# Optimization experiments

Hardware: AMD Instinct MI355X
Metric: run time of the kernel (lower is better)

Reference implementation:

```python
import jax, jax.numpy as jnp
import numpy as np


def _relative_position_index(ws: int) -> np.ndarray:
    # Matches torch meshgrid (ij) construction in _init_relative_positions.
    coords = np.stack(np.meshgrid(np.arange(ws), np.arange(ws), indexing='ij'), axis=0).reshape(2, -1)  # [2, ws*ws]
    rel = coords[:, :, None] - coords[:, None, :]          # [2, N, N]
    rel = rel.transpose(1, 2, 0).copy()                    # [N, N, 2]
    rel[:, :, 0] += ws - 1
    rel[:, :, 1] += ws - 1
    rel[:, :, 0] *= 2 * ws - 1
    return rel.sum(-1)                                     # [N, N] int


def setup_inputs() -> dict:
    key = jax.random.key(0)
    ks = jax.random.split(key, 6)
    B, N, C, H, WS = 4096, 49, 512, 16, 7
    x = jax.random.normal(ks[0], (B, N, C), dtype=jnp.float32)
    w_qkv = jax.random.normal(ks[1], (C, 3 * C), dtype=jnp.float32) * (C ** -0.5)
    b_qkv = jax.random.normal(ks[2], (3 * C,), dtype=jnp.float32) * 0.02
    w_proj = jax.random.normal(ks[3], (C, C), dtype=jnp.float32) * (C ** -0.5)
    b_proj = jax.random.normal(ks[4], (C,), dtype=jnp.float32) * 0.02
    bias_table = jax.random.normal(ks[5], ((2 * WS - 1) ** 2, H), dtype=jnp.float32) * 0.02
    return {"x": x, "w_qkv": w_qkv, "b_qkv": b_qkv, "w_proj": w_proj,
            "b_proj": b_proj, "bias_table": bias_table,
            "num_heads": H, "window_size": WS}


def reference(x, w_qkv, b_qkv, w_proj, b_proj, bias_table, num_heads, window_size):
    B, N, C = x.shape
    hd = C // num_heads
    qkv = (x @ w_qkv + b_qkv).reshape(B, N, 3, num_heads, hd)
    q, k, v = (qkv[:, :, i].transpose(0, 2, 1, 3) for i in range(3))  # each [B, H, N, hd]
    # NOTE: scale uses full channel dim C (as in source), not head_dim.
    attn = jnp.einsum('bhnd,bhmd->bhnm', q, k) * (C ** -0.5)          # [B, H, N, N]
    idx = _relative_position_index(window_size)                        # [N, N] static
    rel_bias = bias_table[idx].transpose(2, 0, 1)                      # [H, N, N]
    attn = jax.nn.softmax(attn + rel_bias[None], axis=-1)
    out = jnp.einsum('bhnm,bhmd->bhnd', attn, v)                       # [B, H, N, hd]
    out = out.transpose(0, 2, 1, 3).reshape(B, N, C)
    return out @ w_proj + b_proj
```

## Files before the change

### kernel.cpp

```cpp
#include <hip/hip_runtime.h>
#include <hip/hip_bf16.h>

typedef __attribute__((ext_vector_type(8))) short bf16x8;
typedef __attribute__((ext_vector_type(4))) float f32x4;

#define DEVI __device__ __forceinline__

DEVI short f2bf(float f) {
  union { float f; unsigned u; } v; v.f = f;
  unsigned r = v.u + 0x7FFFu + ((v.u >> 16) & 1u);
  return (short)(r >> 16);
}

DEVI void gl16(const void* g, void* l) {
  __builtin_amdgcn_global_load_lds((const __attribute__((address_space(1))) unsigned*)g,
                                   (__attribute__((address_space(3))) unsigned*)l,
                                   16, 0, 0);
}

DEVI float exp2a(float x) { float r; asm("v_exp_f32 %0, %1" : "=v"(r) : "v"(x)); return r; }

DEVI unsigned pk2(float lo, float hi) {
  union { __hip_bfloat162 h; unsigned u; } v;
  float2 f; f.x = lo; f.y = hi;
  v.h = __float22bfloat162_rn(f);
  return v.u;
}

union U8 { unsigned u[4]; bf16x8 v; };
DEVI bf16x8 mk8(unsigned a, unsigned b, unsigned c, unsigned d) {
  U8 x; x.u[0]=a; x.u[1]=b; x.u[2]=c; x.u[3]=d; return x.v;
}


__global__ __launch_bounds__(256) void conv_x_k(const float* __restrict__ x,
                                                short* __restrict__ xb) {
  long i = (long)blockIdx.x * 256 + threadIdx.x;
  const float4* xf = (const float4*)x;
  float4 a = xf[i * 2], c = xf[i * 2 + 1];
  bf16x8 r;
  r[0] = f2bf(a.x); r[1] = f2bf(a.y); r[2] = f2bf(a.z); r[3] = f2bf(a.w);
  r[4] = f2bf(c.x); r[5] = f2bf(c.y); r[6] = f2bf(c.z); r[7] = f2bf(c.w);
  *(bf16x8*)(xb + i * 8) = r;
}

__global__ __launch_bounds__(256) void conv_wT_k(const float* __restrict__ w,
                                                 short* __restrict__ wT, int Ncols) {
  int i = blockIdx.x * 256 + threadIdx.x;
  if (i >= Ncols * 512) return;
  int n = i >> 9, k = i & 511;
  wT[i] = f2bf(w[k * Ncols + n]);
}

__global__ __launch_bounds__(256) void fill_biasT(const float* __restrict__ btab,
                                                  float* __restrict__ biasT) {
  int i = blockIdx.x * 256 + threadIdx.x;
  int h = i >> 12, m = (i >> 6) & 63, n = i & 63;
  float v;
  if (m >= 49) {
    v = -1e30f;
  } else {
    int nn = n > 48 ? 48 : n;
    int ni = nn / 7, nj = nn - ni * 7;
    int mi = m / 7,  mj = m - mi * 7;
    int idx = (ni - mi + 6) * 13 + (nj - mj + 6);
    v = btab[idx * 16 + h] * 1.4426950408889634f;
  }
  biasT[i] = v;
}


template <int EPI>
__global__ __launch_bounds__(512, 2)
void gemm256(const short* __restrict__ A, const short* __restrict__ Bt,
             const float* __restrict__ bias, void* __restrict__ outp, int ctiles) {
  __shared__ short Ls[65536];

  const int nwg = gridDim.x;
  const int w = blockIdx.x;
  const int chunk = nwg >> 3;
  const int tid = (w & 7) * chunk + (w >> 3);
  const int rt = tid / ctiles, ct = tid % ctiles;
  const long m0 = (long)rt * 256;
  const int n0 = ct * 256;

  const int t = threadIdx.x;
  const int lane = t & 63;
  const int wv = t >> 6;
  const int wr = wv >> 2;
  const int wc = wv & 3;
  const int l15 = lane & 15, g = lane >> 4;

  const int srow = t >> 3;
  const int gch = (t & 7) ^ (srow & 7);
  const short* Ag = A + (m0 + srow) * 512 + gch * 8;
  const short* Bg = Bt + (long)(n0 + srow) * 512 + gch * 8;

  const int x7 = l15 & 7;
  const int c0 = (g ^ x7) * 8;
  const int c1 = ((4 + g) ^ x7) * 8;
  const int rA64 = (wr * 128 + l15) * 64;
  const int rB64 = (wc * 64 + l15) * 64 + 16384;

  f32x4 acc[8][4] = {};

  {
    short* Ad = Ls + t * 8;
    short* Bd = Ls + 16384 + t * 8;
#pragma unroll
    for (int s2 = 0; s2 < 4; ++s2) {
      gl16(Ag + s2 * 32768, Ad + s2 * 4096);
      gl16(Bg + s2 * 32768, Bd + s2 * 4096);
    }
  }
  __syncthreads();

  for (int kt = 0; kt < 8; ++kt) {
    const int cur = kt & 1;
    const short* Ab = Ls + cur * 32768;
    short* Ad = Ls + (cur ^ 1) * 32768 + t * 8;
    short* Bd = Ad + 16384;
    const short* Agk = Ag + (kt + 1) * 64;
    const short* Bgk = Bg + (kt + 1) * 64;

    bf16x8 af[8], bf[4];

#pragma unroll
    for (int mf = 0; mf < 8; ++mf) af[mf] = *(const bf16x8*)(Ab + rA64 + mf * 1024 + c0);
#pragma unroll
    for (int nf = 0; nf < 4; ++nf) bf[nf] = *(const bf16x8*)(Ab + rB64 + nf * 1024 + c0);
    if (kt < 7) {
#pragma unroll
      for (int s2 = 0; s2 < 4; ++s2) gl16(Agk + s2 * 32768, Ad + s2 * 4096);
    }
#pragma unroll
    for (int mf = 0; mf < 8; ++mf)
#pragma unroll
      for (int nf = 0; nf < 4; ++nf)
        acc[mf][nf] = __builtin_amdgcn_mfma_f32_16x16x32_bf16(af[mf], bf[nf], acc[mf][nf], 0, 0, 0);

#pragma unroll
    for (int mf = 0; mf < 8; ++mf) af[mf] = *(const bf16x8*)(Ab + rA64 + mf * 1024 + c1);
#pragma unroll
    for (int nf = 0; nf < 4; ++nf) bf[nf] = *(const bf16x8*)(Ab + rB64 + nf * 1024 + c1);
    if (kt < 7) {
#pragma unroll
      for (int s2 = 0; s2 < 4; ++s2) gl16(Bgk + s2 * 32768, Bd + s2 * 4096);
    }
#pragma unroll
    for (int mf = 0; mf < 8; ++mf)
#pragma unroll
      for (int nf = 0; nf < 4; ++nf)
        acc[mf][nf] = __builtin_amdgcn_mfma_f32_16x16x32_bf16(af[mf], bf[nf], acc[mf][nf], 0, 0, 0);

    __syncthreads();
  }

  if (EPI == 0) {
    short* qkv = (short*)outp;
#pragma unroll
    for (int mf = 0; mf < 8; ++mf)
#pragma unroll
      for (int r = 0; r < 4; ++r) {
        int row = (int)m0 + wr * 128 + mf * 16 + g * 4 + r;
        int b = row / 49, n = row - b * 49;
#pragma unroll
        for (int nf = 0; nf < 4; ++nf) {
          int col = n0 + wc * 64 + nf * 16 + l15;
          float val = acc[mf][nf][r] + bias[col];
          int ii = col >> 9, h = (col >> 5) & 15, d = col & 31;
          qkv[(long)((b * 16 + h) * 3 + ii) * 1568 + n * 32 + d] = f2bf(val);
        }
      }
  } else {
    float* out = (float*)outp;
#pragma unroll
    for (int mf = 0; mf < 8; ++mf)
#pragma unroll
      for (int r = 0; r < 4; ++r) {
        long row = m0 + wr * 128 + mf * 16 + g * 4 + r;
#pragma unroll
        for (int nf = 0; nf < 4; ++nf) {
          int col = n0 + wc * 64 + nf * 16 + l15;
          out[row * 512 + col] = acc[mf][nf][r] + bias[col];
        }
      }
  }
}


__global__ __launch_bounds__(256, 3)
void attn49(const short* __restrict__ qkvb, const float* __restrict__ biasT,
            short* __restrict__ ao) {
  const int t = threadIdx.x, lane = t & 63, wv = t >> 6;
  const int l15 = lane & 15, g = lane >> 4, g4 = g * 4;
  const int b = blockIdx.x >> 2;
  const int h = (blockIdx.x & 3) * 4 + wv;

  const short* qb = qkvb + (long)(b * 16 + h) * 3 * 1568;
  const short* kb = qb + 1568;
  const short* vb = kb + 1568;

  bf16x8 qf[4], kf[4];
#pragma unroll
  for (int i = 0; i < 4; ++i) {
    int row = i * 16 + l15; row = row > 48 ? 48 : row;
    kf[i] = *(const bf16x8*)(kb + row * 32 + g * 8);
    qf[i] = *(const bf16x8*)(qb + row * 32 + g * 8);
  }

  bf16x8 vf[2][2];
#pragma unroll
  for (int kt = 0; kt < 2; ++kt)
#pragma unroll
    for (int hi = 0; hi < 2; ++hi)
#pragma unroll
      for (int r = 0; r < 4; ++r) {
        int m = kt * 32 + hi * 16 + g4 + r;
        m = m > 48 ? 48 : m;
#pragma unroll
        for (int dt = 0; dt < 2; ++dt)
          vf[kt][dt][hi * 4 + r] = vb[m * 32 + dt * 16 + l15];
      }

  f32x4 s[4][4] = {};
#pragma unroll
  for (int i = 0; i < 4; ++i)
#pragma unroll
    for (int j = 0; j < 4; ++j)
      s[i][j] = __builtin_amdgcn_mfma_f32_16x16x32_bf16(kf[i], qf[j], s[i][j], 0, 0, 0);

  const float* biasH = biasT + h * 4096;
  float sum[4] = {0.f, 0.f, 0.f, 0.f};
#pragma unroll
  for (int i = 0; i < 4; ++i)
#pragma unroll
    for (int r = 0; r < 4; ++r) {
      int m = i * 16 + g4 + r;
      const float* bp = biasH + m * 64 + l15;
#pragma unroll
      for (int j = 0; j < 4; ++j) {
        float p = exp2a(fmaf(s[i][j][r], 0.06375871f, bp[j * 16]));
        s[i][j][r] = p;
        sum[j] += p;
      }
    }
#pragma unroll
  for (int j = 0; j < 4; ++j) {
    sum[j] += __shfl_xor(sum[j], 16);
    sum[j] += __shfl_xor(sum[j], 32);
    sum[j] = 1.f / sum[j];
  }

  unsigned pk[4][4][2];
#pragma unroll
  for (int j = 0; j < 4; ++j)
#pragma unroll
    for (int i = 0; i < 4; ++i) {
      pk[j][i][0] = pk2(s[i][j][0] * sum[j], s[i][j][1] * sum[j]);
      pk[j][i][1] = pk2(s[i][j][2] * sum[j], s[i][j][3] * sum[j]);
    }

  f32x4 o[4][2] = {};
#pragma unroll
  for (int j = 0; j < 4; ++j) {
    bf16x8 a0 = mk8(pk[j][0][0], pk[j][0][1], pk[j][1][0], pk[j][1][1]);
    bf16x8 a1 = mk8(pk[j][2][0], pk[j][2][1], pk[j][3][0], pk[j][3][1]);
    o[j][0] = __builtin_amdgcn_mfma_f32_16x16x32_bf16(a0, vf[0][0], o[j][0], 0, 0, 0);
    o[j][0] = __builtin_amdgcn_mfma_f32_16x16x32_bf16(a1, vf[1][0], o[j][0], 0, 0, 0);
    o[j][1] = __builtin_amdgcn_mfma_f32_16x16x32_bf16(a0, vf[0][1], o[j][1], 0, 0, 0);
    o[j][1] = __builtin_amdgcn_mfma_f32_16x16x32_bf16(a1, vf[1][1], o[j][1], 0, 0, 0);
  }

#pragma unroll
  for (int j = 0; j < 4; ++j)
#pragma unroll
    for (int r = 0; r < 4; ++r) {
      int n = j * 16 + g4 + r;
      if (n < 49) {
        long off = ((long)b * 49 + n) * 512 + h * 32 + l15;
        ao[off]      = f2bf(o[j][0][r]);
        ao[off + 16] = f2bf(o[j][1][r]);
      }
    }
}


extern "C" void kernel_launch(void* const* d_in, const int* in_sizes, int n_in,
                              void* d_out, int out_size, void* d_ws, size_t ws_size,
                              hipStream_t stream) {
  (void)in_sizes; (void)n_in; (void)out_size; (void)ws_size;
  const float* x      = (const float*)d_in[0];
  const float* w_qkv  = (const float*)d_in[1];
  const float* b_qkv  = (const float*)d_in[2];
  const float* w_proj = (const float*)d_in[3];
  const float* b_proj = (const float*)d_in[4];
  const float* btab   = (const float*)d_in[5];

  char* ws = (char*)d_ws;
  short* xb  = (short*)ws;
  short* wqT = (short*)(ws + 205520896L);
  short* wpT = (short*)(ws + 205520896L + 1572864L);
  short* qkv = (short*)(ws + 205520896L + 1572864L + 524288L);
  short* ao  = xb;
  float* biasT = (float*)wqT;

  conv_x_k <<<50176, 256, 0, stream>>>(x, xb);
  conv_wT_k<<<3072, 256, 0, stream>>>(w_qkv, wqT, 1536);
  conv_wT_k<<<1024, 256, 0, stream>>>(w_proj, wpT, 512);
  gemm256<0><<<4704, 512, 0, stream>>>(xb, wqT, b_qkv, (void*)qkv, 6);
  fill_biasT<<<256, 256, 0, stream>>>(btab, biasT);
  attn49   <<<16384, 256, 0, stream>>>(qkv, biasT, ao);
  gemm256<1><<<1568, 512, 0, stream>>>(ao, wpT, b_proj, d_out, 2);
}
```

Baseline: 958.0 us.

## Restructure GEMM main loop into fine-grained staged pipeline with barriers and setprio

Rewrites the 256x256 GEMM k-loop so each k-tile is split into two 32-wide halves stored as separate LDS sub-tiles with a new 4-chunk XOR swizzle. Global-to-LDS loads for the next tile are interleaved with four MFMA phases, using explicit s_barrier, vmcnt waits and s_setprio to raise MFMA issue priority. The intent is better overlap of memory traffic with matrix math and fewer LDS bank conflicts. The risks are the extra barriers per iteration and a subtle correctness hazard in the vmcnt counting, since the final iteration re-stages tile 7.

```diff
diff --git a/kernel.cpp b/kernel.cpp
--- a/kernel.cpp
+++ b/kernel.cpp
@@ -91,69 +91,69 @@
   const int wc = wv & 3;
   const int l15 = lane & 15, g = lane >> 4;
 
-  const int srow = t >> 3;
-  const int gch = (t & 7) ^ (srow & 7);
-  const short* Ag = A + (m0 + srow) * 512 + gch * 8;
-  const short* Bg = Bt + (long)(n0 + srow) * 512 + gch * 8;
-
-  const int x7 = l15 & 7;
-  const int c0 = (g ^ x7) * 8;
-  const int c1 = ((4 + g) ^ x7) * 8;
-  const int rA64 = (wr * 128 + l15) * 64;
-  const int rB64 = (wc * 64 + l15) * 64 + 16384;
+  const int gch = (t & 3) ^ ((t >> 3) & 3);
+  const short* Ag = A + (m0 + (t >> 2)) * 512 + gch * 8;
+  const short* Bg = Bt + (long)(n0 + (t >> 2)) * 512 + gch * 8;
+
+  const int cA = ((g ^ ((l15 >> 1) & 3))) * 8;
+  const int rowA = (wr * 128 + l15) * 32;
+  const int rowB = (wc * 64 + l15) * 32;
 
   f32x4 acc[8][4] = {};
-
-  {
-    short* Ad = Ls + t * 8;
-    short* Bd = Ls + 16384 + t * 8;
-#pragma unroll
-    for (int s2 = 0; s2 < 4; ++s2) {
-      gl16(Ag + s2 * 32768, Ad + s2 * 4096);
-      gl16(Bg + s2 * 32768, Bd + s2 * 4096);
-    }
-  }
-  __syncthreads();
+  bf16x8 af[8], bfr[2];
+
+#define STAGE_A(ktn, kh, bufn)                                         \
+  { const short* s_ = Ag + (ktn) * 64 + (kh) * 32;                     \
+    short* d_ = (bufn) + (kh) * 8192 + t * 8;                          \
+    gl16(s_, d_); gl16(s_ + 128 * 512, d_ + 4096); }
+#define STAGE_B(ktn, kh, bufn)                                         \
+  { const short* s_ = Bg + (ktn) * 64 + (kh) * 32;                     \
+    short* d_ = (bufn) + 16384 + (kh) * 8192 + t * 8;                  \
+    gl16(s_, d_); gl16(s_ + 128 * 512, d_ + 4096); }
+#define LOAD_AF(Ab, kh)                                                \
+  _Pragma("unroll")                                                    \
+  for (int mf = 0; mf < 8; ++mf)                                       \
+    af[mf] = *(const bf16x8*)((Ab) + (kh) * 8192 + rowA + mf * 512 + cA);
+#define LOAD_BF(Ab, kh, nh)                                            \
+  bfr[0] = *(const bf16x8*)((Ab) + 16384 + (kh) * 8192 + rowB + ((nh) * 2) * 512 + cA); \
+  bfr[1] = *(const bf16x8*)((Ab) + 16384 + (kh) * 8192 + rowB + ((nh) * 2 + 1) * 512 + cA);
+#define MFMA16(nh)                                                     \
+  __builtin_amdgcn_s_setprio(1);                                       \
+  _Pragma("unroll")                                                    \
+  for (int mf = 0; mf < 8; ++mf) {                                     \
+    acc[mf][(nh) * 2] = __builtin_amdgcn_mfma_f32_16x16x32_bf16(af[mf], bfr[0], acc[mf][(nh) * 2], 0, 0, 0);         \
+    acc[mf][(nh) * 2 + 1] = __builtin_amdgcn_mfma_f32_16x16x32_bf16(af[mf], bfr[1], acc[mf][(nh) * 2 + 1], 0, 0, 0); \
+  }                                                                    \
+  __builtin_amdgcn_s_setprio(0);
+#define BAR() asm volatile("s_barrier" ::: "memory")
+#define VMW4() asm volatile("s_waitcnt vmcnt(4)" ::: "memory")
+
+  STAGE_A(0, 0, Ls); STAGE_B(0, 0, Ls); STAGE_A(0, 1, Ls); STAGE_B(0, 1, Ls);
+  VMW4();
+  BAR();
 
   for (int kt = 0; kt < 8; ++kt) {
-    const int cur = kt & 1;
-    const short* Ab = Ls + cur * 32768;
-    short* Ad = Ls + (cur ^ 1) * 32768 + t * 8;
-    short* Bd = Ad + 16384;
-    const short* Agk = Ag + (kt + 1) * 64;
-    const short* Bgk = Bg + (kt + 1) * 64;
-
-    bf16x8 af[8], bf[4];
-
-#pragma unroll
-    for (int mf = 0; mf < 8; ++mf) af[mf] = *(const bf16x8*)(Ab + rA64 + mf * 1024 + c0);
-#pragma unroll
-    for (int nf = 0; nf < 4; ++nf) bf[nf] = *(const bf16x8*)(Ab + rB64 + nf * 1024 + c0);
-    if (kt < 7) {
-#pragma unroll
-      for (int s2 = 0; s2 < 4; ++s2) gl16(Agk + s2 * 32768, Ad + s2 * 4096);
-    }
-#pragma unroll
-    for (int mf = 0; mf < 8; ++mf)
-#pragma unroll
-      for (int nf = 0; nf < 4; ++nf)
-        acc[mf][nf] = __builtin_amdgcn_mfma_f32_16x16x32_bf16(af[mf], bf[nf], acc[mf][nf], 0, 0, 0);
-
-#pragma unroll
-    for (int mf = 0; mf < 8; ++mf) af[mf] = *(const bf16x8*)(Ab + rA64 + mf * 1024 + c1);
-#pragma unroll
-    for (int nf = 0; nf < 4; ++nf) bf[nf] = *(const bf16x8*)(Ab + rB64 + nf * 1024 + c1);
-    if (kt < 7) {
-#pragma unroll
-      for (int s2 = 0; s2 < 4; ++s2) gl16(Bgk + s2 * 32768, Bd + s2 * 4096);
-    }
-#pragma unroll
-    for (int mf = 0; mf < 8; ++mf)
-#pragma unroll
-      for (int nf = 0; nf < 4; ++nf)
-        acc[mf][nf] = __builtin_amdgcn_mfma_f32_16x16x32_bf16(af[mf], bf[nf], acc[mf][nf], 0, 0, 0);
-
-    __syncthreads();
+    const short* Ab = Ls + (kt & 1) * 32768;
+    short* Bn = Ls + ((kt & 1) ^ 1) * 32768;
+    const int ktn = kt < 7 ? kt + 1 : 7;
+
+    LOAD_AF(Ab, 0); LOAD_BF(Ab, 0, 0);
+    STAGE_A(ktn, 0, Bn);
+    BAR(); MFMA16(0); BAR();
+
+    LOAD_BF(Ab, 0, 1);
+    STAGE_B(ktn, 0, Bn);
+    VMW4();
+    BAR(); MFMA16(1); BAR();
+
+    LOAD_AF(Ab, 1); LOAD_BF(Ab, 1, 0);
+    STAGE_A(ktn, 1, Bn);
+    BAR(); MFMA16(0); BAR();
+
+    LOAD_BF(Ab, 1, 1);
+    STAGE_B(ktn, 1, Bn);
+    VMW4();
+    BAR(); MFMA16(1); BAR();
   }
 
   if (EPI == 0) {
@@ -186,6 +186,13 @@
         }
       }
   }
+#undef STAGE_A
+#undef STAGE_B
+#undef LOAD_AF
+#undef LOAD_BF
+#undef MFMA16
+#undef BAR
+#undef VMW4
 }
 
 
```

New measurement: 895.2 us. 1.07x faster.
